# Kernel optimization log

Hardware: AMD Instinct MI355X
Metric: run time of the kernel (lower is better)

Reference implementation:

```python
import jax, jax.numpy as jnp
import numpy as np

N = 100_000      # nodes
E = 1_600_000    # edges
EMB = 128        # embedding_size
H = 128          # h_feats
G = 128          # graphs in batch
L = 4            # SAGEConv layers
EPS = 1e-5       # batchnorm eps


def setup_inputs() -> dict:
    key = jax.random.key(0)
    ks = jax.random.split(key, 11)
    in_feat = jax.random.randint(ks[0], (N,), 0, 257)
    src = jax.random.randint(ks[1], (E,), 0, N)
    dst = jax.random.randint(ks[2], (E,), 0, N)
    graph_ids = jnp.sort(jax.random.randint(ks[3], (N,), 0, G))
    s = 1.0 / np.sqrt(H)
    emb = jax.random.normal(ks[4], (257, EMB), jnp.float32) * 0.02
    W_self = jax.random.normal(ks[5], (L, H, H), jnp.float32) * s
    W_neigh = jax.random.normal(ks[6], (L, H, H), jnp.float32) * s
    b = jax.random.normal(ks[7], (L, H), jnp.float32) * 0.01
    gamma = jnp.ones((L, H), jnp.float32)
    beta = jnp.zeros((L, H), jnp.float32)
    prelu_w = jnp.full((L, H), 0.25, jnp.float32)
    return dict(in_feat=in_feat, src=src, dst=dst, graph_ids=graph_ids,
                emb=emb, W_self=W_self, W_neigh=W_neigh, b=b,
                gamma=gamma, beta=beta, prelu_w=prelu_w)


def reference(in_feat, src, dst, graph_ids, emb, W_self, W_neigh, b, gamma, beta, prelu_w):
    n = in_feat.shape[0]
    h = emb[in_feat]  # [N, EMB]
    ones_e = jnp.ones(src.shape[0], h.dtype)
    deg = jnp.clip(jax.ops.segment_sum(ones_e, dst, num_segments=n), 1.0)  # in-degree
    outs = []
    for l in range(L):
        # mean neighbor aggregation (src -> dst)
        agg = jax.ops.segment_sum(h[src], dst, num_segments=n) / deg[:, None]
        rst = h @ W_self[l] + agg @ W_neigh[l] + b[l]
        # PReLU (per-channel), then BatchNorm1d (training-mode batch stats), per DGL SAGEConv order
        rst = jnp.where(rst > 0, rst, prelu_w[l] * rst)
        mu = rst.mean(0)
        var = rst.var(0)
        rst = (rst - mu) * jax.lax.rsqrt(var + EPS) * gamma[l] + beta[l]
        outs.append(rst)
        h = rst
    hcat = jnp.concatenate(outs, axis=1)  # [N, 4H]
    cnt = jnp.clip(jax.ops.segment_sum(jnp.ones(n, hcat.dtype), graph_ids, num_segments=G), 1.0)
    g_vec = jax.ops.segment_sum(hcat, graph_ids, num_segments=G) / cnt[:, None]  # [G, 4H]
    return g_vec
```

## Files before the change

### kernel.cpp

```cpp
#include <hip/hip_runtime.h>
#include <hip/hip_bf16.h>


#define EPS_BN 1e-5f
#define BSH 9
#define BCHUNK 4096
#define PCAP 10240
#define AGG_BLOCKS 2048

typedef __attribute__((ext_vector_type(8))) short bf16x8;
typedef __attribute__((ext_vector_type(4))) float f32x4;
typedef __attribute__((address_space(1))) const void gconst_t;
typedef __attribute__((address_space(3))) void ldsv_t;

__global__ __launch_bounds__(256) void k_embed(const int* __restrict__ feat,
                                               const float* __restrict__ emb,
                                               __hip_bfloat162* __restrict__ hb2, int n) {
  int idx = blockIdx.x * 256 + threadIdx.x;
  if (idx < n * 64) {
    int i = idx >> 6, c2 = idx & 63;
    float2 v = ((const float2*)emb)[feat[i] * 64 + c2];
    hb2[idx] = __float22bfloat162_rn(v);
  }
}

__global__ __launch_bounds__(256) void k_wconv(const float* __restrict__ W,
                                               __hip_bfloat16* __restrict__ Wt, int total) {
  int idx = blockIdx.x * 256 + threadIdx.x;
  if (idx < total) {
    int l = idx >> 14, r = idx & 16383, nn = r >> 7, kk = r & 127;
    Wt[idx] = __float2bfloat16(W[(l << 14) + kk * 128 + nn]);
  }
}

__global__ void k_gcount(const int* __restrict__ gid, int* __restrict__ gcnt,
                         int* __restrict__ gstart, int n, int G) {
  int g = blockIdx.x * blockDim.x + threadIdx.x;
  if (g >= G) return;
  int lo0 = 0, hi = n;
  while (lo0 < hi) { int mid = (lo0 + hi) >> 1; if (gid[mid] < g) lo0 = mid + 1; else hi = mid; }
  int lo1 = lo0; hi = n;
  while (lo1 < hi) { int mid = (lo1 + hi) >> 1; if (gid[mid] < g + 1) lo1 = mid + 1; else hi = mid; }
  gstart[g] = lo0;
  gcnt[g] = lo1 - lo0;
}

__global__ __launch_bounds__(256) void k_bhist(const int* __restrict__ dst,
                                               int* __restrict__ bktcnt, int m, int nbkt) {
  __shared__ int h[256];
  int t = threadIdx.x;
  h[t] = 0;
  __syncthreads();
#pragma unroll
  for (int k = 0; k < 4; ++k) {
    int idx = blockIdx.x * BCHUNK + k * 1024 + t * 4;
    if (idx + 4 <= m) {
      int4 d = *(const int4*)&dst[idx];
      atomicAdd(&h[d.x >> BSH], 1);
      atomicAdd(&h[d.y >> BSH], 1);
      atomicAdd(&h[d.z >> BSH], 1);
      atomicAdd(&h[d.w >> BSH], 1);
    } else {
      for (int e = idx; e < m && e < idx + 4; ++e) atomicAdd(&h[dst[e] >> BSH], 1);
    }
  }
  __syncthreads();
  for (int b = t; b < nbkt; b += 256)
    if (h[b]) atomicAdd(&bktcnt[b], h[b]);
}

__global__ void k_bscan(const int* __restrict__ bktcnt, int* __restrict__ bbase,
                        int* __restrict__ bcur, int m, int nbkt) {
  __shared__ int sh[256];
  int t = threadIdx.x;
  int v = (t < nbkt) ? bktcnt[t] : 0;
  sh[t] = v;
  __syncthreads();
  for (int o = 1; o < 256; o <<= 1) {
    int x = (t >= o) ? sh[t - o] : 0;
    __syncthreads();
    sh[t] += x;
    __syncthreads();
  }
  if (t < nbkt) { bbase[t] = sh[t] - v; bcur[t] = sh[t] - v; }
  if (t == 0) bbase[nbkt] = m;
}

__global__ __launch_bounds__(256) void k_bin(const int* __restrict__ src, const int* __restrict__ dst,
                                             int* __restrict__ bcur, uint2* __restrict__ binned,
                                             int m, int nbkt) {
  __shared__ uint2 st[BCHUNK];
  __shared__ int bcnt[256], boff[256], bres[256], wcur[256], ss[256];
  int t = threadIdx.x;
  int e0 = blockIdx.x * BCHUNK;
  int cn = min(BCHUNK, m - e0);
  int sv[16], dv[16];
  for (int b = t; b < 256; b += 256) bcnt[b] = 0;
  __syncthreads();
#pragma unroll
  for (int k = 0; k < 16; ++k) {
    int idx = e0 + k * 256 + t;
    if (idx < e0 + cn) {
      sv[k] = src[idx];
      dv[k] = dst[idx];
      atomicAdd(&bcnt[dv[k] >> BSH], 1);
    } else dv[k] = -1;
  }
  __syncthreads();
  int v = (t < nbkt) ? bcnt[t] : 0;
  ss[t] = v;
  __syncthreads();
  for (int o = 1; o < 256; o <<= 1) {
    int x = (t >= o) ? ss[t - o] : 0;
    __syncthreads();
    ss[t] += x;
    __syncthreads();
  }
  if (t < nbkt) {
    int ex = ss[t] - v;
    boff[t] = ex;
    wcur[t] = ex;
    if (v) bres[t] = atomicAdd(&bcur[t], v);
  }
  __syncthreads();
#pragma unroll
  for (int k = 0; k < 16; ++k) {
    if (dv[k] >= 0) {
      int b = dv[k] >> BSH;
      int p = atomicAdd(&wcur[b], 1);
      st[p] = make_uint2((unsigned)sv[k], (unsigned)dv[k]);
    }
  }
  __syncthreads();
  for (int j = t; j < cn; j += 256) {
    uint2 e = st[j];
    int b = (int)(e.y >> BSH);
    binned[(size_t)bres[b] + (j - boff[b])] = e;
  }
}

__global__ __launch_bounds__(256) void k_cnt(const uint2* __restrict__ binned,
                                             const int* __restrict__ bbase,
                                             int* __restrict__ cnt, int n) {
  __shared__ int h[512];
  int b = blockIdx.x, t = threadIdx.x;
  int base = b << BSH;
  int nn = min(512, n - base);
  h[t] = 0; h[t + 256] = 0;
  __syncthreads();
  int lo = bbase[b], hi = bbase[b + 1];
  for (int j = lo + t; j < hi; j += 256) atomicAdd(&h[(int)binned[j].y - base], 1);
  __syncthreads();
  if (t < nn) cnt[base + t] = h[t];
  if (t + 256 < nn) cnt[base + t + 256] = h[t + 256];
}

__global__ __launch_bounds__(256) void k_scan1(const int* __restrict__ cnt,
                                               int* __restrict__ excl,
                                               int* __restrict__ blk_sums, int n) {
  __shared__ int sh[256];
  int t = threadIdx.x;
  int base = blockIdx.x * 1024 + t * 4;
  int4 v = {0, 0, 0, 0};
  if (base < n) v = *(const int4*)&cnt[base];
  int s = v.x + v.y + v.z + v.w;
  sh[t] = s;
  __syncthreads();
  for (int off = 1; off < 256; off <<= 1) {
    int x = (t >= off) ? sh[t - off] : 0;
    __syncthreads();
    sh[t] += x;
    __syncthreads();
  }
  int ex = sh[t] - s;
  if (t == 255) blk_sums[blockIdx.x] = sh[255];
  if (base < n) {
    excl[base]     = ex;
    excl[base + 1] = ex + v.x;
    excl[base + 2] = ex + v.x + v.y;
    excl[base + 3] = ex + v.x + v.y + v.z;
  }
}

__global__ void k_scan2(int* __restrict__ bs, int nb) {
  __shared__ int sh[128];
  int t = threadIdx.x;
  int v = (t < nb) ? bs[t] : 0;
  sh[t] = v;
  __syncthreads();
  for (int off = 1; off < 128; off <<= 1) {
    int x = (t >= off) ? sh[t - off] : 0;
    __syncthreads();
    sh[t] += x;
    __syncthreads();
  }
  if (t < nb) bs[t] = sh[t] - v;
}

__global__ __launch_bounds__(256) void k_scan3(int* __restrict__ rp, const int* __restrict__ bs,
                                               const int* __restrict__ cnt, int* __restrict__ cursor,
                                               float* __restrict__ deg, int n, int ne) {
  int i = blockIdx.x * 256 + threadIdx.x;
  if (i < n) {
    int r = rp[i] + bs[i >> 10];
    rp[i] = r;
    cursor[i] = r;
    int c = cnt[i];
    deg[i] = (float)(c > 0 ? c : 1);
  }
  if (i == 0) rp[n] = ne;
}

__global__ __launch_bounds__(256) void k_place(const uint2* __restrict__ binned,
                                               const int* __restrict__ bbase,
                                               const int* __restrict__ rp,
                                               int* __restrict__ cursor,
                                               int* __restrict__ csr_src, int n) {
  int b = blockIdx.x, t = threadIdx.x;
  int base = b << BSH;
  int lo = bbase[b], hi = bbase[b + 1], m = hi - lo;
  if (m <= 0) return;
  if (m > PCAP) {
    for (int j = lo + t; j < hi; j += 256) {
      uint2 e = binned[j];
      int p = atomicAdd(&cursor[(int)e.y], 1);
      csr_src[p] = (int)e.x;
    }
    return;
  }
  __shared__ int h[512], loff[512], wc[512], ss[256];
  __shared__ int stage[PCAP];
  h[t] = 0; h[t + 256] = 0;
  __syncthreads();
  for (int j = lo + t; j < hi; j += 256) atomicAdd(&h[(int)binned[j].y - base], 1);
  __syncthreads();
  int a0 = h[2 * t], a1 = h[2 * t + 1];
  int s = a0 + a1;
  ss[t] = s;
  __syncthreads();
  for (int o = 1; o < 256; o <<= 1) {
    int x = (t >= o) ? ss[t - o] : 0;
    __syncthreads();
    ss[t] += x;
    __syncthreads();
  }
  int ex = ss[t] - s;
  loff[2 * t] = ex; loff[2 * t + 1] = ex + a0;
  wc[2 * t] = ex;   wc[2 * t + 1] = ex + a0;
  __syncthreads();
  for (int j = lo + t; j < hi; j += 256) {
    uint2 e = binned[j];
    int p = atomicAdd(&wc[(int)e.y - base], 1);
    stage[p] = (int)e.x;
  }
  __syncthreads();
  int cb = rp[base];
  for (int j = t; j < m; j += 256) csr_src[cb + j] = stage[j];
}

__global__ __launch_bounds__(256) void k_prep(const float* __restrict__ b0,
                                              float* __restrict__ ss0,
                                              float* __restrict__ beffS0,
                                              float* __restrict__ cN0,
                                              const uint4* __restrict__ Wst0,
                                              const uint4* __restrict__ Wnt0,
                                              uint4* __restrict__ Ws2,
                                              uint4* __restrict__ Wn2) {
  int id = blockIdx.x * 256 + threadIdx.x;
  if (id < 128) {
    ss0[id] = 1.f; ss0[128 + id] = 0.f;
    beffS0[id] = b0[id]; cN0[id] = 0.f;
  }
  int half = id >> 11, ch = id & 2047;
  if (half) Wn2[ch] = Wnt0[ch]; else Ws2[ch] = Wst0[ch];
}

__global__ __launch_bounds__(256) void k_gemm2(
    const __hip_bfloat16* __restrict__ hb,
    const __hip_bfloat16* __restrict__ Wst2, const __hip_bfloat16* __restrict__ Wnt2,
    __hip_bfloat16* __restrict__ Ys, __hip_bfloat16* __restrict__ Yn, int n) {
  __shared__ short Ah[128 * 128];
  int t = threadIdx.x;
  int row0 = blockIdx.x * 128;
  int w = t >> 6, lane = t & 63;

#pragma unroll
  for (int rd = 0; rd < 8; ++rd) {
    int Gq = rd * 256 + w * 64 + lane;
    int r = Gq >> 4;
    int gq = (Gq & 15) ^ (r & 7);
    int grow = row0 + r;
    grow = grow < n ? grow : n - 1;
    const __hip_bfloat16* gs = hb + (size_t)grow * 128 + gq * 8;
    __builtin_amdgcn_global_load_lds((gconst_t*)gs,
        (ldsv_t*)&Ah[(rd * 256 + w * 64) * 8], 16, 0, 0);
  }
  asm volatile("s_waitcnt vmcnt(0)" ::: "memory");
  __syncthreads();

  int lr16 = lane & 15, hi = lane >> 4;
  const __hip_bfloat16* Bt[2] = {Wst2, Wnt2};
  __hip_bfloat16* Ot[2] = {Ys, Yn};
#pragma unroll
  for (int s = 0; s < 2; ++s) {
    const __hip_bfloat16* B = Bt[s];
    f32x4 acc[2][8];
#pragma unroll
    for (int fm = 0; fm < 2; ++fm)
#pragma unroll
      for (int fn = 0; fn < 8; ++fn) acc[fm][fn] = (f32x4){0.f, 0.f, 0.f, 0.f};
#pragma unroll
    for (int ks = 0; ks < 4; ++ks) {
      bf16x8 af[2], bfr[8];
#pragma unroll
      for (int fm = 0; fm < 2; ++fm) {
        int rl = w * 32 + fm * 16 + lr16;
        int gq = (ks * 4 + hi) ^ (lr16 & 7);
        af[fm] = *(const bf16x8*)&Ah[rl * 128 + gq * 8];
      }
#pragma unroll
      for (int fn = 0; fn < 8; ++fn)
        bfr[fn] = *(const bf16x8*)(B + (size_t)(fn * 16 + lr16) * 128 + ks * 32 + hi * 8);
#pragma unroll
      for (int fm = 0; fm < 2; ++fm)
#pragma unroll
        for (int fn = 0; fn < 8; ++fn)
          acc[fm][fn] = __builtin_amdgcn_mfma_f32_16x16x32_bf16(af[fm], bfr[fn], acc[fm][fn], 0, 0, 0);
    }
    __hip_bfloat16* O = Ot[s];
#pragma unroll
    for (int fm = 0; fm < 2; ++fm) {
      int rbase = row0 + w * 32 + fm * 16 + hi * 4;
#pragma unroll
      for (int fn = 0; fn < 8; ++fn) {
        int col = fn * 16 + lr16;
#pragma unroll
        for (int r = 0; r < 4; ++r) {
          int grow = rbase + r;
          if (grow < n) O[(size_t)grow * 128 + col] = __float2bfloat16(acc[fm][fn][r]);
        }
      }
    }
  }
}

__device__ __forceinline__ void acc8(float* a, uint4 v) {
  float2 f;
  f = __bfloat1622float2(*(const __hip_bfloat162*)&v.x); a[0] += f.x; a[1] += f.y;
  f = __bfloat1622float2(*(const __hip_bfloat162*)&v.y); a[2] += f.x; a[3] += f.y;
  f = __bfloat1622float2(*(const __hip_bfloat162*)&v.z); a[4] += f.x; a[5] += f.y;
  f = __bfloat1622float2(*(const __hip_bfloat162*)&v.w); a[6] += f.x; a[7] += f.y;
}

__global__ __launch_bounds__(256) void k_agg(const uint4* __restrict__ yn4,
                                             const int* __restrict__ rp,
                                             const int* __restrict__ csr_src,
                                             const float* __restrict__ deg,
                                             uint4* __restrict__ aggY4, int n) {
  int lane = threadIdx.x & 63, wid = threadIdx.x >> 6;
  int g = lane >> 4, lr = lane & 15;
  for (int i = blockIdx.x * 4 + wid; i < n; i += gridDim.x * 4) {
    int beg = rp[i], end = rp[i + 1];
    float a[8];
#pragma unroll
    for (int c = 0; c < 8; ++c) a[c] = 0.f;
    int e = beg;
    for (; e + 8 <= end; e += 8) {
      int s0 = csr_src[e + g];
      int s1 = csr_src[e + 4 + g];
      uint4 v0 = yn4[(size_t)s0 * 16 + lr];
      uint4 v1 = yn4[(size_t)s1 * 16 + lr];
      acc8(a, v0);
      acc8(a, v1);
    }
    for (; e + g < end; e += 4) {
      int s = csr_src[e + g];
      uint4 v = yn4[(size_t)s * 16 + lr];
      acc8(a, v);
    }
#pragma unroll
    for (int c = 0; c < 8; ++c) {
      a[c] += __shfl_xor(a[c], 16, 64);
      a[c] += __shfl_xor(a[c], 32, 64);
    }
    if (g == 0) {
      float invd = 1.0f / deg[i];
      __hip_bfloat162 p0 = __float22bfloat162_rn(make_float2(a[0] * invd, a[1] * invd));
      __hip_bfloat162 p1 = __float22bfloat162_rn(make_float2(a[2] * invd, a[3] * invd));
      __hip_bfloat162 p2 = __float22bfloat162_rn(make_float2(a[4] * invd, a[5] * invd));
      __hip_bfloat162 p3 = __float22bfloat162_rn(make_float2(a[6] * invd, a[7] * invd));
      uint4 o;
      o.x = *(unsigned int*)&p0; o.y = *(unsigned int*)&p1;
      o.z = *(unsigned int*)&p2; o.w = *(unsigned int*)&p3;
      aggY4[(size_t)i * 16 + lr] = o;
    }
  }
}

__global__ __launch_bounds__(256) void k_finpool(
    const uint4* __restrict__ ys4, const uint4* __restrict__ aggY4,
    const int* __restrict__ cnt,
    const float* __restrict__ beffS, const float* __restrict__ cN,
    const float* __restrict__ pw,
    const int* __restrict__ gstart, const int* __restrict__ gcnt,
    uint4* __restrict__ hbn4, float* __restrict__ out,
    float* __restrict__ partial, int l, int n) {
  __shared__ float redS[4][128], redQ[4][128];
  int g = blockIdx.x >> 3, c = blockIdx.x & 7;
  int len = gcnt[g];
  int i0 = gstart[g] + ((len * c) >> 3);
  int i1 = gstart[g] + ((len * (c + 1)) >> 3);
  if (i0 >= i1) return;
  int t = threadIdx.x, w = t >> 6, lane = t & 63;
  int gi = lane >> 4, lr = lane & 15;
  float bS[8], cn8[8], pw8[8], S[8], Q[8];
#pragma unroll
  for (int k = 0; k < 8; ++k) {
    bS[k] = beffS[lr * 8 + k];
    cn8[k] = cN[lr * 8 + k];
    pw8[k] = pw[lr * 8 + k];
    S[k] = 0.f; Q[k] = 0.f;
  }
  for (int r = i0 + w * 4 + gi; r < i1; r += 16) {
    uint4 ys = ys4[(size_t)r * 16 + lr];
    uint4 ag = aggY4[(size_t)r * 16 + lr];
    bool has = cnt[r] > 0;
    float y[8], a[8];
    float2 f;
    f = __bfloat1622float2(*(const __hip_bfloat162*)&ys.x); y[0] = f.x; y[1] = f.y;
    f = __bfloat1622float2(*(const __hip_bfloat162*)&ys.y); y[2] = f.x; y[3] = f.y;
    f = __bfloat1622float2(*(const __hip_bfloat162*)&ys.z); y[4] = f.x; y[5] = f.y;
    f = __bfloat1622float2(*(const __hip_bfloat162*)&ys.w); y[6] = f.x; y[7] = f.y;
    f = __bfloat1622float2(*(const __hip_bfloat162*)&ag.x); a[0] = f.x; a[1] = f.y;
    f = __bfloat1622float2(*(const __hip_bfloat162*)&ag.y); a[2] = f.x; a[3] = f.y;
    f = __bfloat1622float2(*(const __hip_bfloat162*)&ag.z); a[4] = f.x; a[5] = f.y;
    f = __bfloat1622float2(*(const __hip_bfloat162*)&ag.w); a[6] = f.x; a[7] = f.y;
    float x[8];
#pragma unroll
    for (int k = 0; k < 8; ++k) {
      float xx = y[k] + bS[k];
      if (has) xx += a[k] + cn8[k];
      xx = xx > 0.f ? xx : pw8[k] * xx;
      S[k] += xx; Q[k] += xx * xx;
      x[k] = xx;
    }
    __hip_bfloat162 p0 = __float22bfloat162_rn(make_float2(x[0], x[1]));
    __hip_bfloat162 p1 = __float22bfloat162_rn(make_float2(x[2], x[3]));
    __hip_bfloat162 p2 = __float22bfloat162_rn(make_float2(x[4], x[5]));
    __hip_bfloat162 p3 = __float22bfloat162_rn(make_float2(x[6], x[7]));
    uint4 o;
    o.x = *(unsigned int*)&p0; o.y = *(unsigned int*)&p1;
    o.z = *(unsigned int*)&p2; o.w = *(unsigned int*)&p3;
    hbn4[(size_t)r * 16 + lr] = o;
  }
#pragma unroll
  for (int k = 0; k < 8; ++k) {
    S[k] += __shfl_xor(S[k], 16, 64);
    S[k] += __shfl_xor(S[k], 32, 64);
    Q[k] += __shfl_xor(Q[k], 16, 64);
    Q[k] += __shfl_xor(Q[k], 32, 64);
  }
  if (gi == 0) {
#pragma unroll
    for (int k = 0; k < 8; ++k) {
      redS[w][lr * 8 + k] = S[k];
      redQ[w][lr * 8 + k] = Q[k];
    }
  }
  __syncthreads();
  if (t < 128) {
    float s = redS[0][t] + redS[1][t] + redS[2][t] + redS[3][t];
    float q = redQ[0][t] + redQ[1][t] + redQ[2][t] + redQ[3][t];
    atomicAdd(&out[(size_t)g * 512 + l * 128 + t], s);
    float* pp = partial + (size_t)(blockIdx.x >> 5) * 256;
    atomicAdd(&pp[t], s);
    atomicAdd(&pp[128 + t], q);
  }
}

__global__ __launch_bounds__(1024) void k_bnfin(float* __restrict__ partial, int nb,
                                                const float* __restrict__ gamma,
                                                const float* __restrict__ beta,
                                                float* __restrict__ ss,
                                                const float* __restrict__ bias_next,
                                                const float* __restrict__ Wsf_next,
                                                const float* __restrict__ Wnf_next,
                                                const __hip_bfloat16* __restrict__ Wst_next,
                                                const __hip_bfloat16* __restrict__ Wnt_next,
                                                __hip_bfloat16* __restrict__ Ws2,
                                                __hip_bfloat16* __restrict__ Wn2,
                                                float* __restrict__ beffS_next,
                                                float* __restrict__ cN_next,
                                                int has_next, int n) {
  __shared__ float red[4][256];
  __shared__ float shv[128], scv[128];
  __shared__ float bredS[8][128], bredN[8][128];
  int t = threadIdx.x, c = t & 255, part = t >> 8;
  float s = 0.f;
  for (int b = part; b < nb; b += 4) s += partial[(size_t)b * 256 + c];
  red[part][c] = s;
  __syncthreads();
  if (part == 0) red[0][c] = red[0][c] + red[1][c] + red[2][c] + red[3][c];
  __syncthreads();
  if (t < 128) {
    float inv_n = 1.0f / (float)n;
    float mu = red[0][t] * inv_n;
    float var = red[0][128 + t] * inv_n - mu * mu;
    float sc = rsqrtf(var + EPS_BN) * gamma[t];
    float sh = beta[t] - mu * sc;
    ss[t] = sc;
    ss[128 + t] = sh;
    shv[t] = sh;
    scv[t] = sc;
  }
  __syncthreads();
  if (has_next) {
    int cc = t & 127, kg = t >> 7;
    float aS = 0.f, aN = 0.f;
#pragma unroll
    for (int k = kg * 16; k < kg * 16 + 16; ++k) {
      float sh = shv[k];
      aS += sh * Wsf_next[k * 128 + cc];
      aN += sh * Wnf_next[k * 128 + cc];
    }
    bredS[kg][cc] = aS;
    bredN[kg][cc] = aN;
    __syncthreads();
    if (t < 128) {
      float rS = bias_next[t], rN = 0.f;
#pragma unroll
      for (int kg2 = 0; kg2 < 8; ++kg2) { rS += bredS[kg2][t]; rN += bredN[kg2][t]; }
      beffS_next[t] = rS;
      cN_next[t] = rN;
    }
    for (int i = t; i < 16384; i += 1024) {
      float scf = scv[i & 127];
      Ws2[i] = __float2bfloat16(__bfloat162float(Wst_next[i]) * scf);
      Wn2[i] = __float2bfloat16(__bfloat162float(Wnt_next[i]) * scf);
    }
  }
  for (int i = t; i < nb * 256; i += 1024) partial[i] = 0.f;
}

__global__ __launch_bounds__(256) void k_div(float* __restrict__ out, const int* __restrict__ gcnt,
                                             const float* __restrict__ ssbuf, int m) {
  int i = blockIdx.x * 256 + threadIdx.x;
  if (i < m) {
    int g = i >> 9;
    int lc = i & 511;
    int l = lc >> 7, c = lc & 127;
    const float* ss = ssbuf + (l + 1) * 256;
    int cn = gcnt[g];
    out[i] = (cn > 0) ? (out[i] / (float)cn) * ss[c] + ss[128 + c] : 0.f;
  }
}

extern "C" void kernel_launch(void* const* d_in, const int* in_sizes, int n_in,
                              void* d_out, int out_size, void* d_ws, size_t ws_size,
                              hipStream_t stream) {
  const int*   in_feat = (const int*)d_in[0];
  const int*   src     = (const int*)d_in[1];
  const int*   dst     = (const int*)d_in[2];
  const int*   gid     = (const int*)d_in[3];
  const float* emb     = (const float*)d_in[4];
  const float* Wself   = (const float*)d_in[5];
  const float* Wneigh  = (const float*)d_in[6];
  const float* bvec    = (const float*)d_in[7];
  const float* gamma   = (const float*)d_in[8];
  const float* beta    = (const float*)d_in[9];
  const float* prelu   = (const float*)d_in[10];
  const int N = in_sizes[0];
  const int E = in_sizes[1];
  const int G = out_size / 512;
  float* out = (float*)d_out;
  const int NB = (N + 127) / 128;
  const int NP = (G * 8 + 31) / 32;
  const int NBKT = (N + 511) >> BSH;

  char* p = (char*)d_ws;
  size_t off = 0;
  auto take = [&](size_t bytes) { void* r = p + off; off += (bytes + 255) & ~(size_t)255; return r; };
  __hip_bfloat16* hb0   = (__hip_bfloat16*)take((size_t)N * 128 * 2);
  __hip_bfloat16* hb1   = (__hip_bfloat16*)take((size_t)N * 128 * 2);
  __hip_bfloat16* Ysb   = (__hip_bfloat16*)take((size_t)N * 128 * 2);
  __hip_bfloat16* Ynb   = (__hip_bfloat16*)take((size_t)N * 128 * 2);
  __hip_bfloat16* Wst   = (__hip_bfloat16*)take((size_t)4 * 128 * 128 * 2);
  __hip_bfloat16* Wnt   = (__hip_bfloat16*)take((size_t)4 * 128 * 128 * 2);
  __hip_bfloat16* Wst2  = (__hip_bfloat16*)take((size_t)128 * 128 * 2);
  __hip_bfloat16* Wnt2  = (__hip_bfloat16*)take((size_t)128 * 128 * 2);
  float* partial        = (float*)take((size_t)NP * 256 * 4);
  float* ssbuf          = (float*)take((size_t)5 * 256 * 4);
  float* beffS          = (float*)take((size_t)4 * 128 * 4);
  float* cNb            = (float*)take((size_t)4 * 128 * 4);
  uint2* binned  = (uint2*)take((size_t)E * 8);
  int*   csr_src = (int*)take((size_t)E * 4);
  int*   cnt     = (int*)take((size_t)N * 4);
  int*   rp      = (int*)take((size_t)(N + 1) * 4);
  int*   cursor  = (int*)take((size_t)N * 4);
  float* deg     = (float*)take((size_t)N * 4);
  int*   bs      = (int*)take(512);
  int*   gcnt    = (int*)take((size_t)G * 4);
  int*   gstart  = (int*)take((size_t)G * 4);
  int*   bktcnt  = (int*)take((size_t)NBKT * 4);
  int*   bbase   = (int*)take((size_t)(NBKT + 1) * 4);
  int*   bcur    = (int*)take((size_t)NBKT * 4);
  if (off > ws_size) return;

  hipMemsetAsync(bktcnt, 0, (size_t)NBKT * 4, stream);
  hipMemsetAsync(partial, 0, (size_t)NP * 256 * 4, stream);
  hipMemsetAsync(d_out, 0, (size_t)out_size * 4, stream);

  k_embed<<<(N * 64 + 255) / 256, 256, 0, stream>>>(in_feat, emb, (__hip_bfloat162*)hb0, N);
  k_wconv<<<(4 * 128 * 128 + 255) / 256, 256, 0, stream>>>(Wself, Wst, 4 * 128 * 128);
  k_wconv<<<(4 * 128 * 128 + 255) / 256, 256, 0, stream>>>(Wneigh, Wnt, 4 * 128 * 128);
  k_gcount<<<1, 128, 0, stream>>>(gid, gcnt, gstart, N, G);

  int nbb = (E + BCHUNK - 1) / BCHUNK;
  k_bhist<<<nbb, 256, 0, stream>>>(dst, bktcnt, E, NBKT);
  k_bscan<<<1, 256, 0, stream>>>(bktcnt, bbase, bcur, E, NBKT);
  k_bin<<<nbb, 256, 0, stream>>>(src, dst, bcur, binned, E, NBKT);
  k_cnt<<<NBKT, 256, 0, stream>>>(binned, bbase, cnt, N);
  int nsb = (N + 1023) / 1024;
  k_scan1<<<nsb, 256, 0, stream>>>(cnt, rp, bs, N);
  k_scan2<<<1, 128, 0, stream>>>(bs, nsb);
  k_scan3<<<(N + 255) / 256, 256, 0, stream>>>(rp, bs, cnt, cursor, deg, N, E);
  k_place<<<NBKT, 256, 0, stream>>>(binned, bbase, rp, cursor, csr_src, N);
  k_prep<<<16, 256, 0, stream>>>(bvec, ssbuf, beffS, cNb,
                                 (const uint4*)Wst, (const uint4*)Wnt,
                                 (uint4*)Wst2, (uint4*)Wnt2);

  __hip_bfloat16* bufs[2] = {hb0, hb1};
  for (int l = 0; l < 4; ++l) {
    __hip_bfloat16* hin  = bufs[l & 1];
    __hip_bfloat16* hout = bufs[(l + 1) & 1];
    k_gemm2<<<NB, 256, 0, stream>>>(hin, Wst2, Wnt2, Ysb, Ynb, N);
    k_agg<<<AGG_BLOCKS, 256, 0, stream>>>((const uint4*)Ynb, rp, csr_src, deg,
                                          (uint4*)hin, N);
    k_finpool<<<G * 8, 256, 0, stream>>>((const uint4*)Ysb, (const uint4*)hin, cnt,
                                         beffS + l * 128, cNb + l * 128,
                                         prelu + l * 128, gstart, gcnt,
                                         (uint4*)hout, out, partial, l, N);
    k_bnfin<<<1, 1024, 0, stream>>>(partial, NP, gamma + l * 128, beta + l * 128,
                                    ssbuf + (l + 1) * 256,
                                    bvec + ((l + 1) & 3) * 128,
                                    Wself + ((l + 1) & 3) * 16384,
                                    Wneigh + ((l + 1) & 3) * 16384,
                                    Wst + ((l + 1) & 3) * 16384,
                                    Wnt + ((l + 1) & 3) * 16384,
                                    Wst2, Wnt2,
                                    beffS + ((l + 1) & 3) * 128,
                                    cNb + ((l + 1) & 3) * 128,
                                    (l < 3) ? 1 : 0, N);
  }
  k_div<<<(out_size + 255) / 256, 256, 0, stream>>>(out, gcnt, ssbuf, out_size);
}
```

Baseline: 596.6 us.

## Vectorize embedding gather, merge weight conversions, unroll aggregation loop deeper

The embedding kernel now has each thread convert 8 floats and write one 16-byte store, instead of one float2 per thread. The two weight-transpose launches are merged into a single launch, saving one kernel launch. The neighbor aggregation loop gains a 16-edge unrolled stage that issues four independent gathers per lane, giving more memory-level parallelism. The deeper unroll raises register pressure, which could lower occupancy.

```diff
diff --git a/kernel.cpp b/kernel.cpp
--- a/kernel.cpp
+++ b/kernel.cpp
@@ -15,22 +15,33 @@
 
 __global__ __launch_bounds__(256) void k_embed(const int* __restrict__ feat,
                                                const float* __restrict__ emb,
-                                               __hip_bfloat162* __restrict__ hb2, int n) {
+                                               uint4* __restrict__ hb4, int n) {
   int idx = blockIdx.x * 256 + threadIdx.x;
-  if (idx < n * 64) {
-    int i = idx >> 6, c2 = idx & 63;
-    float2 v = ((const float2*)emb)[feat[i] * 64 + c2];
-    hb2[idx] = __float22bfloat162_rn(v);
-  }
-}
-
-__global__ __launch_bounds__(256) void k_wconv(const float* __restrict__ W,
-                                               __hip_bfloat16* __restrict__ Wt, int total) {
+  if (idx < n * 16) {
+    int i = idx >> 4, c8 = idx & 15;
+    const float4* e = (const float4*)(emb + (size_t)feat[i] * 128 + c8 * 8);
+    float4 f0 = e[0], f1 = e[1];
+    __hip_bfloat162 p0 = __float22bfloat162_rn(make_float2(f0.x, f0.y));
+    __hip_bfloat162 p1 = __float22bfloat162_rn(make_float2(f0.z, f0.w));
+    __hip_bfloat162 p2 = __float22bfloat162_rn(make_float2(f1.x, f1.y));
+    __hip_bfloat162 p3 = __float22bfloat162_rn(make_float2(f1.z, f1.w));
+    uint4 o;
+    o.x = *(unsigned int*)&p0; o.y = *(unsigned int*)&p1;
+    o.z = *(unsigned int*)&p2; o.w = *(unsigned int*)&p3;
+    hb4[idx] = o;
+  }
+}
+
+__global__ __launch_bounds__(256) void k_wconv(const float* __restrict__ Ws,
+                                               const float* __restrict__ Wn,
+                                               __hip_bfloat16* __restrict__ Wst,
+                                               __hip_bfloat16* __restrict__ Wnt) {
   int idx = blockIdx.x * 256 + threadIdx.x;
-  if (idx < total) {
-    int l = idx >> 14, r = idx & 16383, nn = r >> 7, kk = r & 127;
-    Wt[idx] = __float2bfloat16(W[(l << 14) + kk * 128 + nn]);
-  }
+  int half = idx >> 16, r = idx & 65535;
+  int l = r >> 14, rr = r & 16383, nn = rr >> 7, kk = rr & 127;
+  const float* W = half ? Wn : Ws;
+  __hip_bfloat16* Wt = half ? Wnt : Wst;
+  Wt[r] = __float2bfloat16(W[(l << 14) + kk * 128 + nn]);
 }
 
 __global__ void k_gcount(const int* __restrict__ gid, int* __restrict__ gcnt,
@@ -365,6 +376,20 @@
 #pragma unroll
     for (int c = 0; c < 8; ++c) a[c] = 0.f;
     int e = beg;
+    for (; e + 16 <= end; e += 16) {
+      int s0 = csr_src[e + g];
+      int s1 = csr_src[e + 4 + g];
+      int s2 = csr_src[e + 8 + g];
+      int s3 = csr_src[e + 12 + g];
+      uint4 v0 = yn4[(size_t)s0 * 16 + lr];
+      uint4 v1 = yn4[(size_t)s1 * 16 + lr];
+      uint4 v2 = yn4[(size_t)s2 * 16 + lr];
+      uint4 v3 = yn4[(size_t)s3 * 16 + lr];
+      acc8(a, v0);
+      acc8(a, v1);
+      acc8(a, v2);
+      acc8(a, v3);
+    }
     for (; e + 8 <= end; e += 8) {
       int s0 = csr_src[e + g];
       int s1 = csr_src[e + 4 + g];
@@ -610,9 +635,8 @@
   hipMemsetAsync(partial, 0, (size_t)NP * 256 * 4, stream);
   hipMemsetAsync(d_out, 0, (size_t)out_size * 4, stream);
 
-  k_embed<<<(N * 64 + 255) / 256, 256, 0, stream>>>(in_feat, emb, (__hip_bfloat162*)hb0, N);
-  k_wconv<<<(4 * 128 * 128 + 255) / 256, 256, 0, stream>>>(Wself, Wst, 4 * 128 * 128);
-  k_wconv<<<(4 * 128 * 128 + 255) / 256, 256, 0, stream>>>(Wneigh, Wnt, 4 * 128 * 128);
+  k_embed<<<(N * 16 + 255) / 256, 256, 0, stream>>>(in_feat, emb, (uint4*)hb0, N);
+  k_wconv<<<(2 * 4 * 128 * 128 + 255) / 256, 256, 0, stream>>>(Wself, Wneigh, Wst, Wnt);
   k_gcount<<<1, 128, 0, stream>>>(gid, gcnt, gstart, N, G);
 
   int nbb = (E + BCHUNK - 1) / BCHUNK;
```

Result: faster. 584.9 us (-2.0%).
